# Optimization experiments

Hardware: AMD Instinct MI355X
Metric: run time of the kernel (lower is better)

The kernel has to match this reference:

```python
import jax, jax.numpy as jnp
import numpy as np

N_A, N_B = 50000, 50000
E = 500000
IN, H, OUT, NGRAPHS = 128, 128, 10, 64
# (src_type, dst_type) per edge type, matching metadata[1]
EDGE_TYPES = [(0, 0), (0, 1), (1, 0), (1, 1)]
NUM_LAYERS = 2
NEG_SLOPE = 0.2  # GATConv leaky_relu slope


def setup_inputs() -> dict:
    key = jax.random.key(0)
    ks = jax.random.split(key, 16)
    ei = [jax.random.randint(ks[2 + e], (2, E), 0, 50000).astype(jnp.int32) for e in range(4)]
    return {
        "x_A": jax.random.normal(ks[0], (N_A, IN), jnp.float32),
        "x_B": jax.random.normal(ks[1], (N_B, IN), jnp.float32),
        "ei0": ei[0], "ei1": ei[1], "ei2": ei[2], "ei3": ei[3],
        "batch_A": jnp.sort(jax.random.randint(ks[6], (N_A,), 0, NGRAPHS)).astype(jnp.int32),
        "batch_B": jnp.sort(jax.random.randint(ks[7], (N_B,), 0, NGRAPHS)).astype(jnp.int32),
        "batch_size": NGRAPHS,
        "w_src": jax.random.normal(ks[8], (NUM_LAYERS, 4, IN, H), jnp.float32) * 0.05,
        "w_dst": jax.random.normal(ks[9], (NUM_LAYERS, 4, IN, H), jnp.float32) * 0.05,
        "att_src": jax.random.normal(ks[10], (NUM_LAYERS, 4, H), jnp.float32) * 0.05,
        "att_dst": jax.random.normal(ks[11], (NUM_LAYERS, 4, H), jnp.float32) * 0.05,
        "conv_bias": jax.random.normal(ks[12], (NUM_LAYERS, 4, H), jnp.float32) * 0.05,
        "wc": jax.random.normal(ks[13], (2 * H, OUT), jnp.float32) * 0.05,
        "bc": jax.random.normal(ks[14], (OUT,), jnp.float32) * 0.05,
    }


def gat_conv(x_src, x_dst, edge_index, ws, wd, a_s, a_d, b, num_dst):
    # PyG GATConv, heads=1, add_self_loops=False, aggr='mean'
    h_src = x_src @ ws            # [Ns, H]
    h_dst = x_dst @ wd            # [Nd, H]
    s_src = h_src @ a_s           # [Ns]
    s_dst = h_dst @ a_d           # [Nd]
    src, dst = edge_index[0], edge_index[1]
    score = jax.nn.leaky_relu(s_src[src] + s_dst[dst], NEG_SLOPE)  # [E]
    # segment softmax over destination nodes
    smax = jax.ops.segment_max(score, dst, num_segments=num_dst)
    ex = jnp.exp(score - smax[dst])
    denom = jax.ops.segment_sum(ex, dst, num_segments=num_dst)
    alpha = ex / denom[dst]
    msg = alpha[:, None] * h_src[src]                               # [E, H]
    summed = jax.ops.segment_sum(msg, dst, num_segments=num_dst)
    cnt = jax.ops.segment_sum(jnp.ones_like(alpha), dst, num_segments=num_dst)
    return summed / jnp.maximum(cnt, 1.0)[:, None] + b


def mean_pool(x, batch, batch_size):
    s = jax.ops.segment_sum(x, batch, num_segments=batch_size)
    c = jax.ops.segment_sum(jnp.ones((x.shape[0],), x.dtype), batch, num_segments=batch_size)
    return s / jnp.maximum(c, 1.0)[:, None]


def reference(x_A, x_B, ei0, ei1, ei2, ei3, batch_A, batch_B, batch_size,
              w_src, w_dst, att_src, att_dst, conv_bias, wc, bc):
    xs = [x_A, x_B]
    eis = [ei0, ei1, ei2, ei3]
    for L in range(NUM_LAYERS):
        outs = {0: [], 1: []}
        for e, (st, dt) in enumerate(EDGE_TYPES):
            o = gat_conv(xs[st], xs[dt], eis[e], w_src[L, e], w_dst[L, e],
                         att_src[L, e], att_dst[L, e], conv_bias[L, e], xs[dt].shape[0])
            outs[dt].append(o)
        # HeteroConv inter_aggr='mean' across edge types, then relu (dropout is identity in eval)
        xs = [jax.nn.relu(jnp.mean(jnp.stack(outs[t], 0), 0)) for t in (0, 1)]
    pooled = [mean_pool(xs[0], batch_A, batch_size), mean_pool(xs[1], batch_B, batch_size)]
    graph_emb = jnp.concatenate(pooled, axis=1)  # [B, 2H]
    return graph_emb @ wc + bc
```

## Files before the change

kernel.cpp:

```cpp
#include <hip/hip_runtime.h>
#include <hip/hip_bf16.h>

#define NN 50000
#define EE 500000
#define GG 64
#define NSL 50
#define SPAN 1000
#define NCH 125
#define EPG (EE / NCH)
#define NCNT (4 * NSL * NCH)
#define SCB ((NCNT + 255) / 256)

typedef __attribute__((ext_vector_type(8))) short bf16x8;
typedef __attribute__((ext_vector_type(4))) float f32x4;

__device__ __forceinline__ float wred_sum(float v) {
#pragma unroll
  for (int s = 32; s; s >>= 1) v += __shfl_xor(v, s, 64);
  return v;
}
__device__ __forceinline__ float gred_sum(float v) {
  v += __shfl_xor(v, 1, 64);
  v += __shfl_xor(v, 2, 64);
  v += __shfl_xor(v, 4, 64);
  v += __shfl_xor(v, 8, 64);
  return v;
}

__device__ __forceinline__ short f2bf(float x) {
  __hip_bfloat16 b = __float2bfloat16(x);
  return *reinterpret_cast<short*>(&b);
}
__device__ __forceinline__ float bf2f(unsigned short s) {
  __hip_bfloat16 b = *reinterpret_cast<__hip_bfloat16*>(&s);
  return __bfloat162float(b);
}

__global__ __launch_bounds__(256) void v_kernel(const float* wdst, const float* adst, float* v) {
  int wv = (blockIdx.x * 256 + threadIdx.x) >> 6;
  int lane = threadIdx.x & 63;
  int le = wv >> 7, k = wv & 127;
  const float* W = wdst + (size_t)le * 16384 + k * 128;
  const float* a = adst + le * 128;
  float p = W[lane] * a[lane] + W[64 + lane] * a[64 + lane];
  p = wred_sum(p);
  if (lane == 0) v[le * 128 + k] = p;
}

__global__ __launch_bounds__(256) void wcvt_kernel(const float* wsrc, short* whiT, short* wloT) {
  int idx = blockIdx.x * 256 + threadIdx.x;
  int le = idx >> 14, rem = idx & 16383;
  int c = rem >> 7, k = rem & 127;
  float v = wsrc[(size_t)le * 16384 + k * 128 + c];
  short hi = f2bf(v);
  whiT[idx] = hi;
  wloT[idx] = f2bf(v - bf2f((unsigned short)hi));
}


__global__ __launch_bounds__(256) void pcount_kernel(const int* e0, const int* e1, const int* e2,
                                                     const int* e3, int* counts) {
  int t = blockIdx.y, ch = blockIdx.x;
  const int* ei = (t == 0 ? e0 : t == 1 ? e1 : t == 2 ? e2 : e3);
  const int* dst = ei + EE;
  __shared__ int cnt[NSL];
  for (int i = threadIdx.x; i < NSL; i += 256) cnt[i] = 0;
  __syncthreads();
  int i0 = ch * EPG;
  for (int i = i0 + threadIdx.x; i < i0 + EPG; i += 256) atomicAdd(&cnt[dst[i] / SPAN], 1);
  __syncthreads();
  for (int sl = threadIdx.x; sl < NSL; sl += 256) counts[(t * NSL + sl) * NCH + ch] = cnt[sl];
}

__global__ __launch_bounds__(256) void scan1_kernel(const int* counts, int* bsums) {
  int tid = threadIdx.x, lane = tid & 63, wid = tid >> 6;
  int idx = blockIdx.x * 256 + tid;
  int v = (idx < NCNT) ? counts[idx] : 0;
#pragma unroll
  for (int s = 32; s; s >>= 1) v += __shfl_xor(v, s, 64);
  __shared__ int ws[4];
  if (lane == 0) ws[wid] = v;
  __syncthreads();
  if (tid == 0) bsums[blockIdx.x] = ws[0] + ws[1] + ws[2] + ws[3];
}

__global__ void scan2_kernel(int* bsums) {
  __shared__ int s[SCB];
  int tid = threadIdx.x;
  if (tid < SCB) s[tid] = bsums[tid];
  __syncthreads();
  if (tid == 0) {
    int run = 0;
    for (int i = 0; i < SCB; i++) { int x = s[i]; s[i] = run; run += x; }
  }
  __syncthreads();
  if (tid < SCB) bsums[tid] = s[tid];
}

__global__ __launch_bounds__(256) void scan3_kernel(int* counts, const int* bsums, int* sliceptr) {
  int tid = threadIdx.x, lane = tid & 63, wid = tid >> 6;
  int idx = blockIdx.x * 256 + tid;
  int v = (idx < NCNT) ? counts[idx] : 0;
  int orig = v;
#pragma unroll
  for (int s = 1; s < 64; s <<= 1) { int u = __shfl_up(v, s, 64); if (lane >= s) v += u; }
  __shared__ int ws[4];
  if (lane == 63) ws[wid] = v;
  __syncthreads();
  int woff = (wid > 0 ? ws[0] : 0) + (wid > 1 ? ws[1] : 0) + (wid > 2 ? ws[2] : 0);
  int excl = bsums[blockIdx.x] + woff + v - orig;
  if (idx < NCNT) {
    counts[idx] = excl;
    if (idx % NCH == 0) {
      int g = idx / NCH;
      sliceptr[(g / NSL) * (NSL + 1) + (g % NSL)] = excl;
    }
  }
  if (blockIdx.x == 0 && tid < 4) sliceptr[tid * (NSL + 1) + NSL] = (tid + 1) * EE;
}

__global__ __launch_bounds__(256) void ppart_kernel(const int* e0, const int* e1, const int* e2,
                                                    const int* e3, const int* counts, int2* pairs) {
  int t = blockIdx.y, ch = blockIdx.x;
  const int* ei = (t == 0 ? e0 : t == 1 ? e1 : t == 2 ? e2 : e3);
  const int* srcr = ei;
  const int* dstr = ei + EE;
  __shared__ int cur[NSL];
  for (int i = threadIdx.x; i < NSL; i += 256) cur[i] = counts[(t * NSL + i) * NCH + ch];
  __syncthreads();
  int i0 = ch * EPG;
  for (int i = i0 + threadIdx.x; i < i0 + EPG; i += 256) {
    int d = dstr[i], s = srcr[i];
    int pos = atomicAdd(&cur[d / SPAN], 1);
    pairs[pos] = make_int2(s, d);
  }
}

__global__ __launch_bounds__(256) void pbuild_kernel(const int2* pairs, const int* sliceptr,
                                                     int* rowptr, int* col) {
  int t = blockIdx.y, sl = blockIdx.x;
  int n0 = sl * SPAN;
  int e0 = sliceptr[t * (NSL + 1) + sl], e1 = sliceptr[t * (NSL + 1) + sl + 1];
  int tid = threadIdx.x, lane = tid & 63, wid = tid >> 6;
  __shared__ int cnt[SPAN];
  __shared__ int wsum[4];
  for (int i = tid; i < SPAN; i += 256) cnt[i] = 0;
  __syncthreads();
  for (int e = e0 + tid; e < e1; e += 256) atomicAdd(&cnt[pairs[e].y - n0], 1);
  __syncthreads();
  int s0 = 0, s1 = 0, s2 = 0, s3 = 0, tot = 0;
  if (tid < SPAN / 4) {
    s0 = cnt[tid * 4]; s1 = cnt[tid * 4 + 1]; s2 = cnt[tid * 4 + 2]; s3 = cnt[tid * 4 + 3];
    tot = s0 + s1 + s2 + s3;
  }
  int v = tot;
#pragma unroll
  for (int sft = 1; sft < 64; sft <<= 1) { int u = __shfl_up(v, sft, 64); if (lane >= sft) v += u; }
  if (lane == 63) wsum[wid] = v;
  __syncthreads();
  int woffv = (wid > 0 ? wsum[0] : 0) + (wid > 1 ? wsum[1] : 0) + (wid > 2 ? wsum[2] : 0);
  int excl = v + woffv - tot;
  __syncthreads();
  if (tid < SPAN / 4) {
    cnt[tid * 4] = excl;
    cnt[tid * 4 + 1] = excl + s0;
    cnt[tid * 4 + 2] = excl + s0 + s1;
    cnt[tid * 4 + 3] = excl + s0 + s1 + s2;
  }
  __syncthreads();
  int base = e0 - t * EE;
  for (int n = tid; n < SPAN; n += 256) rowptr[(size_t)t * (NN + 1) + n0 + n] = base + cnt[n];
  if (sl == NSL - 1 && tid == 0) rowptr[(size_t)t * (NN + 1) + NN] = EE;
  __syncthreads();
  int* ct = col + (size_t)t * EE;
  for (int e = e0 + tid; e < e1; e += 256) {
    int2 p = pairs[e];
    int pos = base + atomicAdd(&cnt[p.y - n0], 1);
    ct[pos] = p.x;
  }
}

__global__ void gbound_kernel(const int* batchA, const int* batchB, int* gbA, int* gbB) {
  int t = threadIdx.x;
  if (t >= 130) return;
  int which = t / 65, g = t % 65;
  const int* b = which ? batchB : batchA;
  int* gb = which ? gbB : gbA;
  int lo = 0, hi = NN;
  while (lo < hi) { int mid = (lo + hi) >> 1; if (b[mid] < g) lo = mid + 1; else hi = mid; }
  gb[g] = lo;
}

#define SWZ(row, kb) ((((row) << 6) + (kb)) ^ (((row) & 7) << 4))
#define HSTRIDE 136

__device__ __forceinline__ void cvt8(const float4 a, const float4 b, bf16x8& hv, bf16x8& lv) {
  short h;
  h = f2bf(a.x); hv[0] = h; lv[0] = f2bf(a.x - bf2f((unsigned short)h));
  h = f2bf(a.y); hv[1] = h; lv[1] = f2bf(a.y - bf2f((unsigned short)h));
  h = f2bf(a.z); hv[2] = h; lv[2] = f2bf(a.z - bf2f((unsigned short)h));
  h = f2bf(a.w); hv[3] = h; lv[3] = f2bf(a.w - bf2f((unsigned short)h));
  h = f2bf(b.x); hv[4] = h; lv[4] = f2bf(b.x - bf2f((unsigned short)h));
  h = f2bf(b.y); hv[5] = h; lv[5] = f2bf(b.y - bf2f((unsigned short)h));
  h = f2bf(b.z); hv[6] = h; lv[6] = f2bf(b.z - bf2f((unsigned short)h));
  h = f2bf(b.w); hv[7] = h; lv[7] = f2bf(b.w - bf2f((unsigned short)h));
}

template <bool XBF>
__global__ __launch_bounds__(256) void gemm_hs_kernel(
    const void* X0_, const void* X1_,
    const short* whiT, const short* wloT,
    const float* attsrc,
    unsigned short* h4, float* s4) {
  int e = blockIdx.z;
  const void* X = (e < 2) ? X0_ : X1_;
  const short* Wh = whiT + (size_t)e * 16384;
  const short* Wl = wloT + (size_t)e * 16384;
  const float* att = attsrc + e * 128;
  unsigned short* h = h4 + (size_t)e * NN * 128;
  float* s_ = s4 + (size_t)e * NN;

  __shared__ short smem[16384];
  short* Ah = smem;
  short* Al = smem + 4096;
  short* Bh = smem + 8192;
  short* Bl = smem + 12288;

  int tid = threadIdx.x;
  int l = tid & 63, w = tid >> 6;
  int arow = l & 15;
  int kb = (l >> 4) << 4;
  int row0 = blockIdx.x * 128;

  f32x4 acc[2][8];
#pragma unroll
  for (int i = 0; i < 2; i++)
#pragma unroll
    for (int j = 0; j < 8; j++) acc[i][j] = (f32x4){0.f, 0.f, 0.f, 0.f};

  float attr[8];
#pragma unroll
  for (int j = 0; j < 8; j++) attr[j] = att[j * 16 + arow];

  int sr = tid >> 1, half = tid & 1;
  int xrow = row0 + sr; xrow = xrow < NN ? xrow : NN - 1;
  const float* xbaseF = nullptr;
  const short* xbaseH = nullptr;
  if constexpr (XBF) xbaseH = (const short*)X + (size_t)xrow * 128 + half * 16;
  else               xbaseF = (const float*)X + (size_t)xrow * 128 + half * 16;
  const short* whbase = Wh + sr * 128 + half * 16;
  const short* wlbase = Wl + sr * 128 + half * 16;
  int soff0 = SWZ(sr, half * 32);
  int soff1 = SWZ(sr, half * 32 + 16);

  float4 f0, f1, f2, f3;
  bf16x8 xh0, xh1;
  if constexpr (XBF) {
    xh0 = *(const bf16x8*)(xbaseH);
    xh1 = *(const bf16x8*)(xbaseH + 8);
  } else {
    f0 = *(const float4*)(xbaseF);
    f1 = *(const float4*)(xbaseF + 4);
    f2 = *(const float4*)(xbaseF + 8);
    f3 = *(const float4*)(xbaseF + 12);
  }
  bf16x8 wh0 = *(const bf16x8*)(whbase);
  bf16x8 wh1 = *(const bf16x8*)(whbase + 8);
  bf16x8 wl0 = *(const bf16x8*)(wlbase);
  bf16x8 wl1 = *(const bf16x8*)(wlbase + 8);

  for (int kt = 0; kt < 128; kt += 32) {
    if constexpr (XBF) {
      *(bf16x8*)((char*)Ah + soff0) = xh0;
      *(bf16x8*)((char*)Ah + soff1) = xh1;
    } else {
      bf16x8 hv0, lv0, hv1, lv1;
      cvt8(f0, f1, hv0, lv0);
      cvt8(f2, f3, hv1, lv1);
      *(bf16x8*)((char*)Ah + soff0) = hv0;
      *(bf16x8*)((char*)Ah + soff1) = hv1;
      *(bf16x8*)((char*)Al + soff0) = lv0;
      *(bf16x8*)((char*)Al + soff1) = lv1;
    }
    *(bf16x8*)((char*)Bh + soff0) = wh0;
    *(bf16x8*)((char*)Bh + soff1) = wh1;
    *(bf16x8*)((char*)Bl + soff0) = wl0;
    *(bf16x8*)((char*)Bl + soff1) = wl1;
    __syncthreads();

    if (kt < 96) {
      if constexpr (XBF) {
        xh0 = *(const bf16x8*)(xbaseH + kt + 32);
        xh1 = *(const bf16x8*)(xbaseH + kt + 40);
      } else {
        f0 = *(const float4*)(xbaseF + kt + 32);
        f1 = *(const float4*)(xbaseF + kt + 36);
        f2 = *(const float4*)(xbaseF + kt + 40);
        f3 = *(const float4*)(xbaseF + kt + 44);
      }
      wh0 = *(const bf16x8*)(whbase + kt + 32);
      wh1 = *(const bf16x8*)(whbase + kt + 40);
      wl0 = *(const bf16x8*)(wlbase + kt + 32);
      wl1 = *(const bf16x8*)(wlbase + kt + 40);
    }

    bf16x8 ah[2], al[2];
#pragma unroll
    for (int i = 0; i < 2; i++) {
      int row = w * 32 + i * 16 + arow;
      ah[i] = *(bf16x8*)((char*)Ah + SWZ(row, kb));
      if constexpr (!XBF) al[i] = *(bf16x8*)((char*)Al + SWZ(row, kb));
    }
#pragma unroll
    for (int j = 0; j < 8; j++) {
      int colr = j * 16 + arow;
      bf16x8 bh = *(bf16x8*)((char*)Bh + SWZ(colr, kb));
      bf16x8 bl = *(bf16x8*)((char*)Bl + SWZ(colr, kb));
#pragma unroll
      for (int i = 0; i < 2; i++) {
        acc[i][j] = __builtin_amdgcn_mfma_f32_16x16x32_bf16(ah[i], bh, acc[i][j], 0, 0, 0);
        acc[i][j] = __builtin_amdgcn_mfma_f32_16x16x32_bf16(ah[i], bl, acc[i][j], 0, 0, 0);
        if constexpr (!XBF)
          acc[i][j] = __builtin_amdgcn_mfma_f32_16x16x32_bf16(al[i], bh, acc[i][j], 0, 0, 0);
      }
    }
    __syncthreads();
  }

#pragma unroll
  for (int p = 0; p < 2; p++) {
    if ((w >> 1) == p) {
#pragma unroll
      for (int i = 0; i < 2; i++) {
#pragma unroll
        for (int r = 0; r < 4; r++) {
          int lrow = (w & 1) * 32 + i * 16 + ((l >> 4) << 2) + r;
          int row = row0 + p * 64 + lrow;
          float pp = 0.f;
#pragma unroll
          for (int j = 0; j < 8; j++) pp += acc[i][j][r] * attr[j];
          pp += __shfl_xor(pp, 1, 64);
          pp += __shfl_xor(pp, 2, 64);
          pp += __shfl_xor(pp, 4, 64);
          pp += __shfl_xor(pp, 8, 64);
          if (row < NN && arow == 0) s_[row] = pp;
#pragma unroll
          for (int j = 0; j < 8; j++) smem[lrow * HSTRIDE + j * 16 + arow] = f2bf(acc[i][j][r]);
        }
      }
    }
    __syncthreads();
#pragma unroll
    for (int it = 0; it < 4; it++) {
      int idx = it * 256 + tid;
      int lrow = idx >> 4, c8 = idx & 15;
      int row = row0 + p * 64 + lrow;
      if (row < NN)
        *(bf16x8*)(h + (size_t)row * 128 + c8 * 8) = *(const bf16x8*)(smem + lrow * HSTRIDE + c8 * 8);
    }
    __syncthreads();
  }
}

#define ACC8(a, uv, wv)                             \
  do {                                              \
    a[0] += wv * __uint_as_float(uv.x << 16);       \
    a[1] += wv * __uint_as_float(uv.x & 0xffff0000u); \
    a[2] += wv * __uint_as_float(uv.y << 16);       \
    a[3] += wv * __uint_as_float(uv.y & 0xffff0000u); \
    a[4] += wv * __uint_as_float(uv.z << 16);       \
    a[5] += wv * __uint_as_float(uv.z & 0xffff0000u); \
    a[6] += wv * __uint_as_float(uv.w << 16);       \
    a[7] += wv * __uint_as_float(uv.w & 0xffff0000u); \
  } while (0)

template <bool XBF>
__global__ __launch_bounds__(256) void agg_kernel(
    const void* xdst_,
    const int* rpA, const int* colA, const unsigned short* hA_, const float* sA_, const float* vA, const float* bA,
    const int* rpB, const int* colB, const unsigned short* hB_, const float* sB_, const float* vB, const float* bB,
    unsigned short* Y) {
  int lane = threadIdx.x & 63;
  int q = lane & 15;
  int gb = lane & 48;
  int t = (lane >> 4) & 1;
  int node = blockIdx.x * 8 + (threadIdx.x >> 5);
  if (node >= NN) return;
  int d0 = q * 8;
  float4 xv0, xv1;
  if constexpr (XBF) {
    const unsigned short* xr = (const unsigned short*)xdst_ + (size_t)node * 128 + d0;
    uint4 u = *(const uint4*)xr;
    xv0 = make_float4(__uint_as_float(u.x << 16), __uint_as_float(u.x & 0xffff0000u),
                      __uint_as_float(u.y << 16), __uint_as_float(u.y & 0xffff0000u));
    xv1 = make_float4(__uint_as_float(u.z << 16), __uint_as_float(u.z & 0xffff0000u),
                      __uint_as_float(u.w << 16), __uint_as_float(u.w & 0xffff0000u));
  } else {
    const float* xr = (const float*)xdst_ + (size_t)node * 128 + d0;
    xv0 = *(const float4*)(xr);
    xv1 = *(const float4*)(xr + 4);
  }

  const int* rp = t ? rpB : rpA;
  const int* cl = t ? colB : colA;
  const unsigned short* h = t ? hB_ : hA_;
  const float* ss = t ? sB_ : sA_;
  const float* v = t ? vB : vA;
  const float* b = t ? bB : bA;
  const uint4* hq = (const uint4*)h + q;

  float4 v0 = *(const float4*)(v + d0);
  float4 v1 = *(const float4*)(v + d0 + 4);
  float part = xv0.x * v0.x + xv0.y * v0.y + xv0.z * v0.z + xv0.w * v0.w +
               xv1.x * v1.x + xv1.y * v1.y + xv1.z * v1.z + xv1.w * v1.w;
  float sd = gred_sum(part);

  int start = rp[node], end = rp[node + 1];
  int deg = end - start;

  float dsum = 0.f;
  float a[8] = {0.f, 0.f, 0.f, 0.f, 0.f, 0.f, 0.f, 0.f};

  for (int base2 = start; base2 < end; base2 += 16) {
    int i = base2 + q;
    int src = 0;
    float ex = 0.f;
    if (i < end) {
      src = cl[i];
      float s = ss[src] + sd;
      s = (s >= 0.f) ? s : 0.2f * s;
      ex = __expf(s);
    }
    dsum += ex;
    int cT = min(16, end - base2);
    int j = 0;
    for (; j + 3 < cT; j += 4) {
      int sj0 = __shfl(src, gb + j, 64);     float e0 = __shfl(ex, gb + j, 64);
      int sj1 = __shfl(src, gb + j + 1, 64); float e1 = __shfl(ex, gb + j + 1, 64);
      int sj2 = __shfl(src, gb + j + 2, 64); float e2 = __shfl(ex, gb + j + 2, 64);
      int sj3 = __shfl(src, gb + j + 3, 64); float e3 = __shfl(ex, gb + j + 3, 64);
      uint4 uv0 = hq[(size_t)sj0 * 16];
      uint4 uv1 = hq[(size_t)sj1 * 16];
      uint4 uv2 = hq[(size_t)sj2 * 16];
      uint4 uv3 = hq[(size_t)sj3 * 16];
      ACC8(a, uv0, e0);
      ACC8(a, uv1, e1);
      ACC8(a, uv2, e2);
      ACC8(a, uv3, e3);
    }
    for (; j < cT; j++) {
      int sj = __shfl(src, gb + j, 64);
      float ej = __shfl(ex, gb + j, 64);
      uint4 uv = hq[(size_t)sj * 16];
      ACC8(a, uv, ej);
    }
  }

  float denom = gred_sum(dsum);
  float inv = (deg > 0) ? 0.5f / (denom * (float)deg) : 0.f;
  float outv[8];
#pragma unroll
  for (int k2 = 0; k2 < 8; k2++) outv[k2] = a[k2] * inv + 0.5f * b[d0 + k2];

#pragma unroll
  for (int k2 = 0; k2 < 8; k2++) outv[k2] += __shfl_xor(outv[k2], 16, 64);

  if (!(lane & 16)) {
    bf16x8 o;
#pragma unroll
    for (int k2 = 0; k2 < 8; k2++) o[k2] = f2bf(fmaxf(outv[k2], 0.f));
    *(bf16x8*)(Y + (size_t)node * 128 + d0) = o;
  }
}

__global__ __launch_bounds__(64) void pool_part_kernel(const unsigned short* XA_, const unsigned short* XB_,
                                                       const int* gbA, const int* gbB,
                                                       float* pooled) {
  int t = blockIdx.y, g = blockIdx.x, c = blockIdx.z;
  const unsigned short* X = t ? XB_ : XA_;
  const int* gb = t ? gbB : gbA;
  int n0 = gb[g], n1 = gb[g + 1];
  int d = threadIdx.x * 2;
  float s0 = 0.f, s1 = 0.f;
  for (int node = n0 + c; node < n1; node += 8) {
    unsigned int u = *(const unsigned int*)(X + (size_t)node * 128 + d);
    s0 += __uint_as_float(u << 16);
    s1 += __uint_as_float(u & 0xffff0000u);
  }
  atomicAdd(&pooled[g * 256 + t * 128 + d], s0);
  atomicAdd(&pooled[g * 256 + t * 128 + d + 1], s1);
}

__global__ void final_kernel(const float* pooled, const int* gbA, const int* gbB,
                             const float* wc, const float* bc, float* out) {
  int tid = blockIdx.x * blockDim.x + threadIdx.x;
  if (tid >= GG * 10) return;
  int g = tid / 10, o = tid % 10;
  float invA = 1.f / fmaxf((float)(gbA[g + 1] - gbA[g]), 1.f);
  float invB = 1.f / fmaxf((float)(gbB[g + 1] - gbB[g]), 1.f);
  float acc = bc[o];
  for (int k = 0; k < 256; k++)
    acc += pooled[g * 256 + k] * (k < 128 ? invA : invB) * wc[k * 10 + o];
  out[g * 10 + o] = acc;
}

extern "C" void kernel_launch(void* const* d_in, const int* in_sizes, int n_in,
                              void* d_out, int out_size, void* d_ws, size_t ws_size,
                              hipStream_t stream) {
  const float* xA = (const float*)d_in[0];
  const float* xB = (const float*)d_in[1];
  const int* ei0 = (const int*)d_in[2];
  const int* ei1 = (const int*)d_in[3];
  const int* ei2 = (const int*)d_in[4];
  const int* ei3 = (const int*)d_in[5];
  const int* batchA = (const int*)d_in[6];
  const int* batchB = (const int*)d_in[7];
  const float* wsrc = (const float*)d_in[9];
  const float* wdst = (const float*)d_in[10];
  const float* attsrc = (const float*)d_in[11];
  const float* attdst = (const float*)d_in[12];
  const float* cbias = (const float*)d_in[13];
  const float* wc = (const float*)d_in[14];
  const float* bc = (const float*)d_in[15];
  float* out = (float*)d_out;

  char* ws = (char*)d_ws;
  size_t off = 0;
  auto alloc = [&](size_t bytes) { size_t o = off; off += (bytes + 255) & ~(size_t)255; return o; };
  size_t o_rowptr = alloc((size_t)4 * (NN + 1) * 4);
  size_t o_col    = alloc((size_t)4 * EE * 4);
  size_t o_cnts   = alloc((size_t)NCNT * 4);
  size_t o_bsums  = alloc((size_t)SCB * 4);
  size_t o_slptr  = alloc((size_t)4 * (NSL + 1) * 4);
  size_t o_v      = alloc((size_t)8 * 128 * 4);
  size_t o_whiT   = alloc((size_t)8 * 16384 * 2);
  size_t o_wloT   = alloc((size_t)8 * 16384 * 2);
  size_t o_h4     = alloc((size_t)4 * NN * 128 * 2);
  size_t o_s4     = alloc((size_t)4 * NN * 4);
  size_t o_Xa1    = alloc((size_t)NN * 128 * 2);
  size_t o_Xb1    = alloc((size_t)NN * 128 * 2);
  size_t o_Xa2    = alloc((size_t)NN * 128 * 2);
  size_t o_Xb2    = alloc((size_t)NN * 128 * 2);
  size_t o_pooled = alloc((size_t)GG * 256 * 4);
  size_t o_gb     = alloc((size_t)2 * (GG + 1) * 4);

  int* rowptr = (int*)(ws + o_rowptr);
  int* col = (int*)(ws + o_col);
  int* counts = (int*)(ws + o_cnts);
  int* bsums = (int*)(ws + o_bsums);
  int* sliceptr = (int*)(ws + o_slptr);
  float* vv = (float*)(ws + o_v);
  short* whiT = (short*)(ws + o_whiT);
  short* wloT = (short*)(ws + o_wloT);
  unsigned short* h4 = (unsigned short*)(ws + o_h4);
  float* s4 = (float*)(ws + o_s4);
  int2* pairs = (int2*)(ws + o_h4);
  unsigned short* Xa1 = (unsigned short*)(ws + o_Xa1);
  unsigned short* Xb1 = (unsigned short*)(ws + o_Xb1);
  unsigned short* Xa2 = (unsigned short*)(ws + o_Xa2);
  unsigned short* Xb2 = (unsigned short*)(ws + o_Xb2);
  float* pooled = (float*)(ws + o_pooled);
  int* gbA = (int*)(ws + o_gb);
  int* gbB = gbA + (GG + 1);

  hipMemsetAsync(pooled, 0, (size_t)GG * 256 * 4, stream);

  v_kernel<<<256, 256, 0, stream>>>(wdst, attdst, vv);
  wcvt_kernel<<<512, 256, 0, stream>>>(wsrc, whiT, wloT);
  gbound_kernel<<<1, 192, 0, stream>>>(batchA, batchB, gbA, gbB);
  pcount_kernel<<<dim3(NCH, 4), 256, 0, stream>>>(ei0, ei1, ei2, ei3, counts);
  scan1_kernel<<<SCB, 256, 0, stream>>>(counts, bsums);
  scan2_kernel<<<1, 128, 0, stream>>>(bsums);
  scan3_kernel<<<SCB, 256, 0, stream>>>(counts, bsums, sliceptr);
  ppart_kernel<<<dim3(NCH, 4), 256, 0, stream>>>(ei0, ei1, ei2, ei3, counts, pairs);
  pbuild_kernel<<<dim3(NSL, 4), 256, 0, stream>>>(pairs, sliceptr, rowptr, col);

  int gemm_gx = (NN + 127) / 128;
  int agg_gx = (NN + 7) / 8;

  for (int L = 0; L < 2; L++) {
    if (L == 0)
      gemm_hs_kernel<false><<<dim3(gemm_gx, 1, 4), 256, 0, stream>>>(
          xA, xB, whiT, wloT, attsrc, h4, s4);
    else
      gemm_hs_kernel<true><<<dim3(gemm_gx, 1, 4), 256, 0, stream>>>(
          Xa1, Xb1, whiT + (size_t)4 * 16384, wloT + (size_t)4 * 16384,
          attsrc + 4 * 128, h4, s4);

    unsigned short* Y0 = (L == 0) ? Xa1 : Xa2;
    unsigned short* Y1 = (L == 0) ? Xb1 : Xb2;
    const float* vvL = vv + L * 4 * 128;
    const float* cbL = cbias + L * 4 * 128;

    if (L == 0)
      agg_kernel<false><<<agg_gx, 256, 0, stream>>>(
          xA,
          rowptr + (size_t)0 * (NN + 1), col + (size_t)0 * EE, h4 + (size_t)0 * NN * 128, s4 + (size_t)0 * NN,
          vvL + 0 * 128, cbL + 0 * 128,
          rowptr + (size_t)2 * (NN + 1), col + (size_t)2 * EE, h4 + (size_t)2 * NN * 128, s4 + (size_t)2 * NN,
          vvL + 2 * 128, cbL + 2 * 128, Y0);
    else
      agg_kernel<true><<<agg_gx, 256, 0, stream>>>(
          Xa1,
          rowptr + (size_t)0 * (NN + 1), col + (size_t)0 * EE, h4 + (size_t)0 * NN * 128, s4 + (size_t)0 * NN,
          vvL + 0 * 128, cbL + 0 * 128,
          rowptr + (size_t)2 * (NN + 1), col + (size_t)2 * EE, h4 + (size_t)2 * NN * 128, s4 + (size_t)2 * NN,
          vvL + 2 * 128, cbL + 2 * 128, Y0);

    if (L == 0)
      agg_kernel<false><<<agg_gx, 256, 0, stream>>>(
          xB,
          rowptr + (size_t)1 * (NN + 1), col + (size_t)1 * EE, h4 + (size_t)1 * NN * 128, s4 + (size_t)1 * NN,
          vvL + 1 * 128, cbL + 1 * 128,
          rowptr + (size_t)3 * (NN + 1), col + (size_t)3 * EE, h4 + (size_t)3 * NN * 128, s4 + (size_t)3 * NN,
          vvL + 3 * 128, cbL + 3 * 128, Y1);
    else
      agg_kernel<true><<<agg_gx, 256, 0, stream>>>(
          Xb1,
          rowptr + (size_t)1 * (NN + 1), col + (size_t)1 * EE, h4 + (size_t)1 * NN * 128, s4 + (size_t)1 * NN,
          vvL + 1 * 128, cbL + 1 * 128,
          rowptr + (size_t)3 * (NN + 1), col + (size_t)3 * EE, h4 + (size_t)3 * NN * 128, s4 + (size_t)3 * NN,
          vvL + 3 * 128, cbL + 3 * 128, Y1);
  }

  pool_part_kernel<<<dim3(GG, 2, 8), 64, 0, stream>>>(Xa2, Xb2, gbA, gbB, pooled);
  final_kernel<<<3, 256, 0, stream>>>(pooled, gbA, gbB, wc, bc, out);
}
```

Baseline: 364.9 us.

## Load GEMM MFMA operands directly from global memory instead of LDS staging

```diff
diff --git a/kernel.cpp b/kernel.cpp
--- a/kernel.cpp
+++ b/kernel.cpp
@@ -191,7 +191,6 @@
   gb[g] = lo;
 }
 
-#define SWZ(row, kb) ((((row) << 6) + (kb)) ^ (((row) & 7) << 4))
 #define HSTRIDE 136
 
 __device__ __forceinline__ void cvt8(const float4 a, const float4 b, bf16x8& hv, bf16x8& lv) {
@@ -220,16 +219,12 @@
   unsigned short* h = h4 + (size_t)e * NN * 128;
   float* s_ = s4 + (size_t)e * NN;
 
-  __shared__ short smem[16384];
-  short* Ah = smem;
-  short* Al = smem + 4096;
-  short* Bh = smem + 8192;
-  short* Bl = smem + 12288;
+  __shared__ short smem[64 * HSTRIDE];
 
   int tid = threadIdx.x;
   int l = tid & 63, w = tid >> 6;
   int arow = l & 15;
-  int kb = (l >> 4) << 4;
+  int koff = (l >> 4) * 8;
   int row0 = blockIdx.x * 128;
 
   f32x4 acc[2][8];
@@ -242,80 +237,35 @@
 #pragma unroll
   for (int j = 0; j < 8; j++) attr[j] = att[j * 16 + arow];
 
-  int sr = tid >> 1, half = tid & 1;
-  int xrow = row0 + sr; xrow = xrow < NN ? xrow : NN - 1;
-  const float* xbaseF = nullptr;
-  const short* xbaseH = nullptr;
-  if constexpr (XBF) xbaseH = (const short*)X + (size_t)xrow * 128 + half * 16;
-  else               xbaseF = (const float*)X + (size_t)xrow * 128 + half * 16;
-  const short* whbase = Wh + sr * 128 + half * 16;
-  const short* wlbase = Wl + sr * 128 + half * 16;
-  int soff0 = SWZ(sr, half * 32);
-  int soff1 = SWZ(sr, half * 32 + 16);
-
-  float4 f0, f1, f2, f3;
-  bf16x8 xh0, xh1;
-  if constexpr (XBF) {
-    xh0 = *(const bf16x8*)(xbaseH);
-    xh1 = *(const bf16x8*)(xbaseH + 8);
-  } else {
-    f0 = *(const float4*)(xbaseF);
-    f1 = *(const float4*)(xbaseF + 4);
-    f2 = *(const float4*)(xbaseF + 8);
-    f3 = *(const float4*)(xbaseF + 12);
-  }
-  bf16x8 wh0 = *(const bf16x8*)(whbase);
-  bf16x8 wh1 = *(const bf16x8*)(whbase + 8);
-  bf16x8 wl0 = *(const bf16x8*)(wlbase);
-  bf16x8 wl1 = *(const bf16x8*)(wlbase + 8);
-
+  const float* afp[2];
+  const short* ahp[2];
+#pragma unroll
+  for (int i = 0; i < 2; i++) {
+    int row = row0 + w * 32 + i * 16 + arow;
+    row = row < NN ? row : NN - 1;
+    if constexpr (XBF) ahp[i] = (const short*)X + (size_t)row * 128 + koff;
+    else               afp[i] = (const float*)X + (size_t)row * 128 + koff;
+  }
+  const short* bhp = Wh + (size_t)arow * 128 + koff;
+  const short* blp = Wl + (size_t)arow * 128 + koff;
+
+#pragma unroll
   for (int kt = 0; kt < 128; kt += 32) {
-    if constexpr (XBF) {
-      *(bf16x8*)((char*)Ah + soff0) = xh0;
-      *(bf16x8*)((char*)Ah + soff1) = xh1;
-    } else {
-      bf16x8 hv0, lv0, hv1, lv1;
-      cvt8(f0, f1, hv0, lv0);
-      cvt8(f2, f3, hv1, lv1);
-      *(bf16x8*)((char*)Ah + soff0) = hv0;
-      *(bf16x8*)((char*)Ah + soff1) = hv1;
-      *(bf16x8*)((char*)Al + soff0) = lv0;
-      *(bf16x8*)((char*)Al + soff1) = lv1;
-    }
-    *(bf16x8*)((char*)Bh + soff0) = wh0;
-    *(bf16x8*)((char*)Bh + soff1) = wh1;
-    *(bf16x8*)((char*)Bl + soff0) = wl0;
-    *(bf16x8*)((char*)Bl + soff1) = wl1;
-    __syncthreads();
-
-    if (kt < 96) {
+    bf16x8 ah[2], al[2];
+#pragma unroll
+    for (int i = 0; i < 2; i++) {
       if constexpr (XBF) {
-        xh0 = *(const bf16x8*)(xbaseH + kt + 32);
-        xh1 = *(const bf16x8*)(xbaseH + kt + 40);
+        ah[i] = *(const bf16x8*)(ahp[i] + kt);
       } else {
-        f0 = *(const float4*)(xbaseF + kt + 32);
-        f1 = *(const float4*)(xbaseF + kt + 36);
-        f2 = *(const float4*)(xbaseF + kt + 40);
-        f3 = *(const float4*)(xbaseF + kt + 44);
+        float4 fa = *(const float4*)(afp[i] + kt);
+        float4 fb = *(const float4*)(afp[i] + kt + 4);
+        cvt8(fa, fb, ah[i], al[i]);
       }
-      wh0 = *(const bf16x8*)(whbase + kt + 32);
-      wh1 = *(const bf16x8*)(whbase + kt + 40);
-      wl0 = *(const bf16x8*)(wlbase + kt + 32);
-      wl1 = *(const bf16x8*)(wlbase + kt + 40);
-    }
-
-    bf16x8 ah[2], al[2];
-#pragma unroll
-    for (int i = 0; i < 2; i++) {
-      int row = w * 32 + i * 16 + arow;
-      ah[i] = *(bf16x8*)((char*)Ah + SWZ(row, kb));
-      if constexpr (!XBF) al[i] = *(bf16x8*)((char*)Al + SWZ(row, kb));
     }
 #pragma unroll
     for (int j = 0; j < 8; j++) {
-      int colr = j * 16 + arow;
-      bf16x8 bh = *(bf16x8*)((char*)Bh + SWZ(colr, kb));
-      bf16x8 bl = *(bf16x8*)((char*)Bl + SWZ(colr, kb));
+      bf16x8 bh = *(const bf16x8*)(bhp + (size_t)j * 2048 + kt);
+      bf16x8 bl = *(const bf16x8*)(blp + (size_t)j * 2048 + kt);
 #pragma unroll
       for (int i = 0; i < 2; i++) {
         acc[i][j] = __builtin_amdgcn_mfma_f32_16x16x32_bf16(ah[i], bh, acc[i][j], 0, 0, 0);
@@ -324,7 +274,6 @@
           acc[i][j] = __builtin_amdgcn_mfma_f32_16x16x32_bf16(al[i], bh, acc[i][j], 0, 0, 0);
       }
     }
-    __syncthreads();
   }
 
 #pragma unroll
```

Measured after the change: 446.5 us. 22.4% more time.
